# Optimization experiments

Measured on AMD Instinct MI355X. Metric: run time of the kernel, lower is better.

The kernel has to match this reference:

```python
import jax, jax.numpy as jnp
import numpy as np

B, T, E = 64, 512, 128
NODES, PATHS, OUT = 100000, 200000, 1000
PAD = 1  # padding_idx for node embedding


def setup_inputs() -> dict:
    key = jax.random.key(0)
    ks = jax.random.split(key, 10)
    starts = jax.random.randint(ks[0], (B, T), 0, NODES)
    paths = jax.random.randint(ks[1], (B, T), 0, PATHS)
    ends = jax.random.randint(ks[2], (B, T), 0, NODES)
    length = jax.random.randint(ks[3], (B,), 0, T)
    node_emb = jax.random.normal(ks[4], (NODES, E), dtype=jnp.float32)
    path_emb = jax.random.normal(ks[5], (PATHS, E), dtype=jnp.float32)
    W = jax.random.normal(ks[6], (E, 3 * E), dtype=jnp.float32)
    a = jax.random.normal(ks[7], (E,), dtype=jnp.float32)
    out_W = jax.random.normal(ks[8], (OUT, E), dtype=jnp.float32) * (1.0 / np.sqrt(E))
    out_b = jax.random.normal(ks[9], (OUT,), dtype=jnp.float32) * 0.01
    return dict(starts=starts, paths=paths, ends=ends, length=length,
                node_emb=node_emb, path_emb=path_emb, W=W, a=a,
                out_W=out_W, out_b=out_b)


def reference(starts, paths, ends, length, node_emb, path_emb, W, a, out_W, out_b):
    # padding_idx=1 -> that embedding row is zero
    node_emb = node_emb.at[PAD].set(0.0)
    es = node_emb[starts]          # [B,T,E]
    ep = path_emb[paths]           # [B,T,E]
    ee = node_emb[ends]            # [B,T,E]
    c = jnp.concatenate([es, ep, ee], axis=2)          # [B,T,3E]
    # dropout is identity in eval mode
    x = jnp.tanh(jnp.einsum('ed,btd->bte', W, c))      # [B,T,E]
    z = jax.nn.softmax(x @ a, axis=1)                  # [B,T] softmax over full T
    # original code sums only first length[i] attention weights (no renorm)
    mask = (jnp.arange(T)[None, :] < length[:, None]).astype(x.dtype)  # [B,T]
    v = jnp.einsum('bte,bt->be', x, z * mask)          # [B,E]
    return v @ out_W.T + out_b                          # [B,OUT]
```

## Files before the change

kernel.cpp:

```cpp
#include <hip/hip_runtime.h>
#include <hip/hip_bf16.h>

#define BB     64
#define TT     512
#define EE     128
#define NROWS  (BB * TT)
#define PADIDX 1
#define OUTN   1000

typedef __attribute__((ext_vector_type(8)))  short short8;
typedef __attribute__((ext_vector_type(16))) float f32x16;

__device__ __forceinline__ float tanh_fast(float v) {
    return 1.0f - 2.0f / (__expf(2.0f * v) + 1.0f);
}

__device__ __forceinline__ void split8(float4 a0, float4 a1, short8& hi, short8& lo) {
    float f[8] = {a0.x, a0.y, a0.z, a0.w, a1.x, a1.y, a1.z, a1.w};
#pragma unroll
    for (int i = 0; i < 8; ++i) {
        unsigned u = __float_as_uint(f[i]);
        unsigned r = (u + (0x7fffu + ((u >> 16) & 1u))) & 0xffff0000u;
        hi[i] = (short)(r >> 16);
        lo[i] = (short)(__float_as_uint(f[i] - __uint_as_float(r)) >> 16);
    }
}

__device__ __forceinline__ void gl_lds16(const void* g, void* l) {
    __builtin_amdgcn_global_load_lds((const __attribute__((address_space(1))) void*)g,
                                     (__attribute__((address_space(3))) void*)l, 16, 0, 0);
}

__global__ __launch_bounds__(256)
void k_prep(const float* __restrict__ W, unsigned short* __restrict__ Whg,
            unsigned short* __restrict__ Wlg)
{
    const int id = blockIdx.x * 256 + threadIdx.x;
    const int e  = id & 127;
    const int d  = id >> 7;
    const float v = W[e * 384 + d];
    const int t = d >> 6, k = d & 63;

    unsigned u = __float_as_uint(v);
    unsigned r = (u + (0x7fffu + ((u >> 16) & 1u))) & 0xffff0000u;
    const unsigned short h = (unsigned short)(r >> 16);
    const unsigned short l = (unsigned short)(__float_as_uint(v - __uint_as_float(r)) >> 16);

    const int boff = t * 16384 + e * 128 + ((k * 2) ^ ((e & 7) << 4));
    *(unsigned short*)((char*)Whg + boff) = h;
    *(unsigned short*)((char*)Wlg + boff) = l;
}

__global__ __launch_bounds__(256, 1)
void k_gemm_x(const int* __restrict__ starts, const int* __restrict__ paths,
              const int* __restrict__ ends,
              const float* __restrict__ node_emb, const float* __restrict__ path_emb,
              const unsigned short* __restrict__ Whg, const unsigned short* __restrict__ Wlg,
              const float* __restrict__ a, float* __restrict__ x, float* __restrict__ s)
{
    extern __shared__ char smem[];
    float*          Af      = (float*)smem;
    unsigned short* Wh      = (unsigned short*)(smem + 65536);
    unsigned short* Wl      = (unsigned short*)(smem + 98304);
    int*            idx_lds = (int*)(smem + 131072);
    float*          s_red   = (float*)(smem + 132608);

    const int tid = threadIdx.x;
    const int r0  = blockIdx.x * 128;

    if (tid < 128) {
        idx_lds[0 * 128 + tid] = starts[r0 + tid];
        idx_lds[1 * 128 + tid] = paths [r0 + tid];
        idx_lds[2 * 128 + tid] = ends  [r0 + tid];
    }

    const int lane = tid & 63;
    const int w    = tid >> 6;
    const int wm   = w >> 1;
    const int wn   = w & 1;
    const int fr   = lane & 31;
    const int kh   = lane >> 5;

    f32x16 acc[2][2];
#pragma unroll
    for (int mi = 0; mi < 2; ++mi)
#pragma unroll
        for (int ni = 0; ni < 2; ++ni)
#pragma unroll
            for (int i = 0; i < 16; ++i) acc[mi][ni][i] = 0.0f;

    __syncthreads();

    bool p0[2], p2[2];
#pragma unroll
    for (int mi = 0; mi < 2; ++mi) {
        const int rm = wm * 64 + mi * 32 + fr;
        p0[mi] = (idx_lds[0 * 128 + rm] == PADIDX);
        p2[mi] = (idx_lds[2 * 128 + rm] == PADIDX);
    }

#define ISSUE(T) do {                                                           \
    const int   seg_  = (T) >> 1;                                               \
    const char* embc_ = (const char*)((seg_ == 1) ? path_emb : node_emb);       \
    char*       afb_  = (char*)Af + (((T) & 1) ? 32768 : 0);                    \
    _Pragma("unroll")                                                           \
    for (int it = 0; it < 8; ++it) {                                            \
        const int row_ = w * 32 + it * 4 + (lane >> 4);                         \
        const int idx_ = idx_lds[seg_ * 128 + row_];                            \
        const char* src_ = embc_ + (size_t)idx_ * 512 + ((T) & 1) * 256         \
                         + (((lane & 15) * 16) ^ ((row_ & 7) << 4));            \
        gl_lds16(src_, afb_ + (w * 32 + it * 4) * 256);                         \
    }                                                                           \
    char* whb_ = (char*)Wh + (((T) & 1) ? 16384 : 0);                           \
    char* wlb_ = (char*)Wl + (((T) & 1) ? 16384 : 0);                           \
    _Pragma("unroll")                                                           \
    for (int rr = 0; rr < 4; ++rr) {                                            \
        const int o_ = rr * 4096 + w * 1024;                                    \
        gl_lds16((const char*)Whg + (T) * 16384 + o_ + lane * 16, whb_ + o_);   \
        gl_lds16((const char*)Wlg + (T) * 16384 + o_ + lane * 16, wlb_ + o_);   \
    }                                                                           \
} while (0)

#define COMPUTE(T) do {                                                         \
    const char* afc_ = (const char*)Af + (((T) & 1) ? 32768 : 0);               \
    const char* whc_ = (const char*)Wh + (((T) & 1) ? 16384 : 0);               \
    const char* wlc_ = (const char*)Wl + (((T) & 1) ? 16384 : 0);               \
    _Pragma("unroll")                                                           \
    for (int ksub = 0; ksub < 4; ++ksub) {                                      \
        short8 ah[2], al[2], bh[2], bl[2];                                      \
        _Pragma("unroll")                                                       \
        for (int mi = 0; mi < 2; ++mi) {                                        \
            const int row_ = wm * 64 + mi * 32 + fr;                            \
            const int swz_ = (row_ & 7) << 4;                                   \
            const int k0b_ = ksub * 64 + kh * 32;                               \
            float4 a0 = *(const float4*)(afc_ + row_ * 256 + (k0b_ ^ swz_));    \
            float4 a1 = *(const float4*)(afc_ + row_ * 256 + ((k0b_ + 16) ^ swz_)); \
            const bool pad_ = ((T) < 2) ? p0[mi] : (((T) >= 4) ? p2[mi] : false); \
            if (pad_) { a0 = make_float4(0.f, 0.f, 0.f, 0.f); a1 = a0; }        \
            split8(a0, a1, ah[mi], al[mi]);                                     \
        }                                                                       \
        _Pragma("unroll")                                                       \
        for (int ni = 0; ni < 2; ++ni) {                                        \
            const int e_ = wn * 64 + ni * 32 + fr;                              \
            const int bo_ = e_ * 128 + ((ksub * 32 + kh * 16) ^ ((e_ & 7) << 4)); \
            bh[ni] = *(const short8*)(whc_ + bo_);                              \
            bl[ni] = *(const short8*)(wlc_ + bo_);                              \
        }                                                                       \
        _Pragma("unroll")                                                       \
        for (int mi = 0; mi < 2; ++mi)                                          \
        _Pragma("unroll")                                                       \
        for (int ni = 0; ni < 2; ++ni) {                                        \
            acc[mi][ni] = __builtin_amdgcn_mfma_f32_32x32x16_bf16(ah[mi], bh[ni], acc[mi][ni], 0, 0, 0); \
            acc[mi][ni] = __builtin_amdgcn_mfma_f32_32x32x16_bf16(ah[mi], bl[ni], acc[mi][ni], 0, 0, 0); \
            acc[mi][ni] = __builtin_amdgcn_mfma_f32_32x32x16_bf16(al[mi], bh[ni], acc[mi][ni], 0, 0, 0); \
        }                                                                       \
    }                                                                           \
} while (0)

    ISSUE(0);

#pragma unroll
    for (int t = 0; t < 6; ++t) {
        if (t < 5) {
            ISSUE(t + 1);
            asm volatile("s_waitcnt vmcnt(16)" ::: "memory");
        } else {
            asm volatile("s_waitcnt vmcnt(0)" ::: "memory");
        }
        __builtin_amdgcn_s_barrier();
        __builtin_amdgcn_sched_barrier(0);
        COMPUTE(t);
        asm volatile("s_waitcnt lgkmcnt(0)" ::: "memory");
        __builtin_amdgcn_sched_barrier(0);
        __builtin_amdgcn_s_barrier();
    }

#undef ISSUE
#undef COMPUTE

    const float a0v = a[wn * 64 + fr];
    const float a1v = a[wn * 64 + 32 + fr];

#pragma unroll
    for (int mi = 0; mi < 2; ++mi) {
        float sp[16];
#pragma unroll
        for (int r = 0; r < 16; ++r) sp[r] = 0.0f;
#pragma unroll
        for (int ni = 0; ni < 2; ++ni) {
            const float ac  = (ni == 0) ? a0v : a1v;
            const int   col = wn * 64 + ni * 32 + fr;
#pragma unroll
            for (int r = 0; r < 16; ++r) {
                const int rowl = (r & 3) + 8 * (r >> 2) + 4 * kh;
                const float tv = tanh_fast(acc[mi][ni][r]);
                x[(size_t)(r0 + wm * 64 + mi * 32 + rowl) * EE + col] = tv;
                sp[r] = fmaf(tv, ac, sp[r]);
            }
        }
#pragma unroll
        for (int m = 1; m < 32; m <<= 1)
#pragma unroll
            for (int r = 0; r < 16; ++r) sp[r] += __shfl_xor(sp[r], m, 64);
        if (fr == 0) {
#pragma unroll
            for (int r = 0; r < 16; ++r) {
                const int rowl = (r & 3) + 8 * (r >> 2) + 4 * kh;
                s_red[(wm * 64 + mi * 32 + rowl) * 2 + wn] = sp[r];
            }
        }
    }
    __syncthreads();
    if (tid < 128) s[r0 + tid] = s_red[tid * 2] + s_red[tid * 2 + 1];
}

__global__ __launch_bounds__(256)
void k_attn(const float* __restrict__ s, const int* __restrict__ length,
            const float* __restrict__ x, float* __restrict__ v)
{
    __shared__ float sw[TT];
    __shared__ float red[256];

    const int b   = blockIdx.x >> 2;
    const int ec  = blockIdx.x & 3;
    const int tid = threadIdx.x;

    const float s0 = s[b * TT + tid];
    const float s1 = s[b * TT + 256 + tid];

    red[tid] = fmaxf(s0, s1);
    __syncthreads();
    for (int st = 128; st > 0; st >>= 1) {
        if (tid < st) red[tid] = fmaxf(red[tid], red[tid + st]);
        __syncthreads();
    }
    const float mx = red[0];
    __syncthreads();

    const float e0 = __expf(s0 - mx);
    const float e1 = __expf(s1 - mx);
    red[tid] = e0 + e1;
    __syncthreads();
    for (int st = 128; st > 0; st >>= 1) {
        if (tid < st) red[tid] += red[tid + st];
        __syncthreads();
    }
    const float inv = 1.0f / red[0];
    const int   len = length[b];
    __syncthreads();

    sw[tid]       = (tid < len)       ? e0 * inv : 0.0f;
    sw[tid + 256] = (tid + 256 < len) ? e1 * inv : 0.0f;
    __syncthreads();

    const int e  = ec * 32 + (tid & 31);
    const int tp = tid >> 5;
    const float* xb = x + (size_t)b * TT * EE;
    float acc = 0.0f;
#pragma unroll 8
    for (int t = tp; t < TT; t += 8)
        acc = fmaf(sw[t], xb[(size_t)t * EE + e], acc);

    red[tid] = acc;
    __syncthreads();
    if (tid < 32) {
        float r2 = 0.0f;
#pragma unroll
        for (int k = 0; k < 8; ++k) r2 += red[k * 32 + tid];
        v[b * EE + ec * 32 + tid] = r2;
    }
}

__global__ __launch_bounds__(256)
void k_out(const float* __restrict__ v, const float* __restrict__ out_W,
           const float* __restrict__ out_b, float* __restrict__ out)
{
    const int id = blockIdx.x * 256 + threadIdx.x;
    const int o  = id >> 6;
    const int bb = id & 63;

    const float4* vr = (const float4*)(v + bb * EE);
    const float4* wr = (const float4*)(out_W + o * EE);
    float acc = 0.0f;
#pragma unroll 8
    for (int qq = 0; qq < 32; ++qq) {
        const float4 a4 = vr[qq];
        const float4 b4 = wr[qq];
        acc = fmaf(a4.x, b4.x, acc);
        acc = fmaf(a4.y, b4.y, acc);
        acc = fmaf(a4.z, b4.z, acc);
        acc = fmaf(a4.w, b4.w, acc);
    }
    out[bb * OUTN + o] = acc + out_b[o];
}

extern "C" void kernel_launch(void* const* d_in, const int* in_sizes, int n_in,
                              void* d_out, int out_size, void* d_ws, size_t ws_size,
                              hipStream_t stream)
{
    const int*   starts   = (const int*)d_in[0];
    const int*   paths    = (const int*)d_in[1];
    const int*   ends     = (const int*)d_in[2];
    const int*   length   = (const int*)d_in[3];
    const float* node_emb = (const float*)d_in[4];
    const float* path_emb = (const float*)d_in[5];
    const float* W        = (const float*)d_in[6];
    const float* a        = (const float*)d_in[7];
    const float* out_W    = (const float*)d_in[8];
    const float* out_b    = (const float*)d_in[9];
    float*       out      = (float*)d_out;

    float* x = (float*)d_ws;
    float* s = x + (size_t)NROWS * EE;
    float* v = s + NROWS;
    unsigned short* Whg = (unsigned short*)(v + BB * EE);
    unsigned short* Wlg = Whg + 6 * 8192;

    static const int SMEM = 133632;
    hipFuncSetAttribute((const void*)k_gemm_x,
                        hipFuncAttributeMaxDynamicSharedMemorySize, SMEM);

    k_prep<<<192, 256, 0, stream>>>(W, Whg, Wlg);
    k_gemm_x<<<NROWS / 128, 256, SMEM, stream>>>(starts, paths, ends,
                                                 node_emb, path_emb, Whg, Wlg,
                                                 a, x, s);
    k_attn<<<BB * 4, 256, 0, stream>>>(s, length, x, v);
    k_out<<<(BB * OUTN) / 256, 256, 0, stream>>>(v, out_W, out_b, out);
}
```

Before: 209.0 us.

## Load gathered embeddings and weights straight into registers instead of staging in LDS

The fused gather-GEMM stops staging embedding rows and bf16 weight tiles through LDS with async loads and double buffering. Each wave now owns a 32-column slice of the output over 64 rows, reads the gathered embedding floats and pre-laid-out weight fragments directly from global memory into MFMA registers, and uses a smaller block tile with two blocks per CU. The prep kernel rewrites the weights into MFMA-fragment order to make these direct loads contiguous. The attention kernel's weighted sum now runs only over the first length rows, skipping masked positions; this relies on L2 and cache hits for reuse instead of explicit LDS pipelining.

```diff
diff --git a/kernel.cpp b/kernel.cpp
--- a/kernel.cpp
+++ b/kernel.cpp
@@ -1,5 +1,4 @@
 #include <hip/hip_runtime.h>
-#include <hip/hip_bf16.h>
 
 #define BB     64
 #define TT     512
@@ -26,192 +25,120 @@
     }
 }
 
-__device__ __forceinline__ void gl_lds16(const void* g, void* l) {
-    __builtin_amdgcn_global_load_lds((const __attribute__((address_space(1))) void*)g,
-                                     (__attribute__((address_space(3))) void*)l, 16, 0, 0);
-}
-
 __global__ __launch_bounds__(256)
 void k_prep(const float* __restrict__ W, unsigned short* __restrict__ Whg,
             unsigned short* __restrict__ Wlg)
 {
     const int id = blockIdx.x * 256 + threadIdx.x;
-    const int e  = id & 127;
-    const int d  = id >> 7;
-    const float v = W[e * 384 + d];
-    const int t = d >> 6, k = d & 63;
-
+    const int j  = id & 7;
+    const int l  = (id >> 3) & 63;
+    const int r2 = id >> 9;
+    const int ks = r2 % 24;
+    const int et = r2 / 24;
+    const int e  = et * 32 + (l & 31);
+    const int k  = ks * 16 + (l >> 5) * 8 + j;
+
+    const float v = W[e * 384 + k];
     unsigned u = __float_as_uint(v);
     unsigned r = (u + (0x7fffu + ((u >> 16) & 1u))) & 0xffff0000u;
-    const unsigned short h = (unsigned short)(r >> 16);
-    const unsigned short l = (unsigned short)(__float_as_uint(v - __uint_as_float(r)) >> 16);
-
-    const int boff = t * 16384 + e * 128 + ((k * 2) ^ ((e & 7) << 4));
-    *(unsigned short*)((char*)Whg + boff) = h;
-    *(unsigned short*)((char*)Wlg + boff) = l;
-}
-
-__global__ __launch_bounds__(256, 1)
+    Whg[id] = (unsigned short)(r >> 16);
+    Wlg[id] = (unsigned short)(__float_as_uint(v - __uint_as_float(r)) >> 16);
+}
+
+__global__ __launch_bounds__(256, 2)
 void k_gemm_x(const int* __restrict__ starts, const int* __restrict__ paths,
               const int* __restrict__ ends,
               const float* __restrict__ node_emb, const float* __restrict__ path_emb,
               const unsigned short* __restrict__ Whg, const unsigned short* __restrict__ Wlg,
               const float* __restrict__ a, float* __restrict__ x, float* __restrict__ s)
 {
-    extern __shared__ char smem[];
-    float*          Af      = (float*)smem;
-    unsigned short* Wh      = (unsigned short*)(smem + 65536);
-    unsigned short* Wl      = (unsigned short*)(smem + 98304);
-    int*            idx_lds = (int*)(smem + 131072);
-    float*          s_red   = (float*)(smem + 132608);
-
-    const int tid = threadIdx.x;
-    const int r0  = blockIdx.x * 128;
-
-    if (tid < 128) {
-        idx_lds[0 * 128 + tid] = starts[r0 + tid];
-        idx_lds[1 * 128 + tid] = paths [r0 + tid];
-        idx_lds[2 * 128 + tid] = ends  [r0 + tid];
-    }
-
+    __shared__ float s_red[64][4];
+
+    const int tid  = threadIdx.x;
     const int lane = tid & 63;
     const int w    = tid >> 6;
-    const int wm   = w >> 1;
-    const int wn   = w & 1;
     const int fr   = lane & 31;
     const int kh   = lane >> 5;
-
-    f32x16 acc[2][2];
+    const int r0   = blockIdx.x * 64;
+
+    const char* base[2][3];
+    bool padf[2][3];
+#pragma unroll
+    for (int mi = 0; mi < 2; ++mi) {
+        const int row = r0 + mi * 32 + fr;
+        const int i0 = starts[row], i1 = paths[row], i2 = ends[row];
+        base[mi][0] = (const char*)node_emb + (size_t)i0 * 512 + kh * 32;
+        base[mi][1] = (const char*)path_emb + (size_t)i1 * 512 + kh * 32;
+        base[mi][2] = (const char*)node_emb + (size_t)i2 * 512 + kh * 32;
+        padf[mi][0] = (i0 == PADIDX);
+        padf[mi][1] = false;
+        padf[mi][2] = (i2 == PADIDX);
+    }
+
+    const char* wbh = (const char*)Whg + ((size_t)(w * 24 * 64) + lane) * 16;
+    const char* wbl = (const char*)Wlg + ((size_t)(w * 24 * 64) + lane) * 16;
+
+    f32x16 acc[2];
 #pragma unroll
     for (int mi = 0; mi < 2; ++mi)
 #pragma unroll
-        for (int ni = 0; ni < 2; ++ni)
-#pragma unroll
-            for (int i = 0; i < 16; ++i) acc[mi][ni][i] = 0.0f;
-
-    __syncthreads();
-
-    bool p0[2], p2[2];
-#pragma unroll
-    for (int mi = 0; mi < 2; ++mi) {
-        const int rm = wm * 64 + mi * 32 + fr;
-        p0[mi] = (idx_lds[0 * 128 + rm] == PADIDX);
-        p2[mi] = (idx_lds[2 * 128 + rm] == PADIDX);
-    }
-
-#define ISSUE(T) do {                                                           \
-    const int   seg_  = (T) >> 1;                                               \
-    const char* embc_ = (const char*)((seg_ == 1) ? path_emb : node_emb);       \
-    char*       afb_  = (char*)Af + (((T) & 1) ? 32768 : 0);                    \
-    _Pragma("unroll")                                                           \
-    for (int it = 0; it < 8; ++it) {                                            \
-        const int row_ = w * 32 + it * 4 + (lane >> 4);                         \
-        const int idx_ = idx_lds[seg_ * 128 + row_];                            \
-        const char* src_ = embc_ + (size_t)idx_ * 512 + ((T) & 1) * 256         \
-                         + (((lane & 15) * 16) ^ ((row_ & 7) << 4));            \
-        gl_lds16(src_, afb_ + (w * 32 + it * 4) * 256);                         \
-    }                                                                           \
-    char* whb_ = (char*)Wh + (((T) & 1) ? 16384 : 0);                           \
-    char* wlb_ = (char*)Wl + (((T) & 1) ? 16384 : 0);                           \
-    _Pragma("unroll")                                                           \
-    for (int rr = 0; rr < 4; ++rr) {                                            \
-        const int o_ = rr * 4096 + w * 1024;                                    \
-        gl_lds16((const char*)Whg + (T) * 16384 + o_ + lane * 16, whb_ + o_);   \
-        gl_lds16((const char*)Wlg + (T) * 16384 + o_ + lane * 16, wlb_ + o_);   \
-    }                                                                           \
-} while (0)
-
-#define COMPUTE(T) do {                                                         \
-    const char* afc_ = (const char*)Af + (((T) & 1) ? 32768 : 0);               \
-    const char* whc_ = (const char*)Wh + (((T) & 1) ? 16384 : 0);               \
-    const char* wlc_ = (const char*)Wl + (((T) & 1) ? 16384 : 0);               \
-    _Pragma("unroll")                                                           \
-    for (int ksub = 0; ksub < 4; ++ksub) {                                      \
-        short8 ah[2], al[2], bh[2], bl[2];                                      \
-        _Pragma("unroll")                                                       \
-        for (int mi = 0; mi < 2; ++mi) {                                        \
-            const int row_ = wm * 64 + mi * 32 + fr;                            \
-            const int swz_ = (row_ & 7) << 4;                                   \
-            const int k0b_ = ksub * 64 + kh * 32;                               \
-            float4 a0 = *(const float4*)(afc_ + row_ * 256 + (k0b_ ^ swz_));    \
-            float4 a1 = *(const float4*)(afc_ + row_ * 256 + ((k0b_ + 16) ^ swz_)); \
-            const bool pad_ = ((T) < 2) ? p0[mi] : (((T) >= 4) ? p2[mi] : false); \
-            if (pad_) { a0 = make_float4(0.f, 0.f, 0.f, 0.f); a1 = a0; }        \
-            split8(a0, a1, ah[mi], al[mi]);                                     \
-        }                                                                       \
-        _Pragma("unroll")                                                       \
-        for (int ni = 0; ni < 2; ++ni) {                                        \
-            const int e_ = wn * 64 + ni * 32 + fr;                              \
-            const int bo_ = e_ * 128 + ((ksub * 32 + kh * 16) ^ ((e_ & 7) << 4)); \
-            bh[ni] = *(const short8*)(whc_ + bo_);                              \
-            bl[ni] = *(const short8*)(wlc_ + bo_);                              \
-        }                                                                       \
-        _Pragma("unroll")                                                       \
-        for (int mi = 0; mi < 2; ++mi)                                          \
-        _Pragma("unroll")                                                       \
-        for (int ni = 0; ni < 2; ++ni) {                                        \
-            acc[mi][ni] = __builtin_amdgcn_mfma_f32_32x32x16_bf16(ah[mi], bh[ni], acc[mi][ni], 0, 0, 0); \
-            acc[mi][ni] = __builtin_amdgcn_mfma_f32_32x32x16_bf16(ah[mi], bl[ni], acc[mi][ni], 0, 0, 0); \
-            acc[mi][ni] = __builtin_amdgcn_mfma_f32_32x32x16_bf16(al[mi], bh[ni], acc[mi][ni], 0, 0, 0); \
-        }                                                                       \
-    }                                                                           \
-} while (0)
-
-    ISSUE(0);
-
-#pragma unroll
-    for (int t = 0; t < 6; ++t) {
-        if (t < 5) {
-            ISSUE(t + 1);
-            asm volatile("s_waitcnt vmcnt(16)" ::: "memory");
-        } else {
-            asm volatile("s_waitcnt vmcnt(0)" ::: "memory");
-        }
-        __builtin_amdgcn_s_barrier();
-        __builtin_amdgcn_sched_barrier(0);
-        COMPUTE(t);
-        asm volatile("s_waitcnt lgkmcnt(0)" ::: "memory");
-        __builtin_amdgcn_sched_barrier(0);
-        __builtin_amdgcn_s_barrier();
-    }
-
-#undef ISSUE
-#undef COMPUTE
-
-    const float a0v = a[wn * 64 + fr];
-    const float a1v = a[wn * 64 + 32 + fr];
+        for (int i = 0; i < 16; ++i) acc[mi][i] = 0.0f;
+
+#pragma unroll
+    for (int ks = 0; ks < 24; ++ks) {
+        const int seg = ks >> 3;
+        const int off = (ks & 7) * 64;
+
+        const short8 bh = *(const short8*)(wbh + ks * 1024);
+        const short8 bl = *(const short8*)(wbl + ks * 1024);
+
+        float4 a0[2], a1[2];
+#pragma unroll
+        for (int mi = 0; mi < 2; ++mi) {
+            a0[mi] = *(const float4*)(base[mi][seg] + off);
+            a1[mi] = *(const float4*)(base[mi][seg] + off + 16);
+            if (padf[mi][seg]) {
+                a0[mi] = make_float4(0.f, 0.f, 0.f, 0.f);
+                a1[mi] = a0[mi];
+            }
+        }
+#pragma unroll
+        for (int mi = 0; mi < 2; ++mi) {
+            short8 ah, al;
+            split8(a0[mi], a1[mi], ah, al);
+            acc[mi] = __builtin_amdgcn_mfma_f32_32x32x16_bf16(ah, bh, acc[mi], 0, 0, 0);
+            acc[mi] = __builtin_amdgcn_mfma_f32_32x32x16_bf16(ah, bl, acc[mi], 0, 0, 0);
+            acc[mi] = __builtin_amdgcn_mfma_f32_32x32x16_bf16(al, bh, acc[mi], 0, 0, 0);
+        }
+    }
+
+    const float av = a[w * 32 + fr];
 
 #pragma unroll
     for (int mi = 0; mi < 2; ++mi) {
         float sp[16];
 #pragma unroll
-        for (int r = 0; r < 16; ++r) sp[r] = 0.0f;
-#pragma unroll
-        for (int ni = 0; ni < 2; ++ni) {
-            const float ac  = (ni == 0) ? a0v : a1v;
-            const int   col = wn * 64 + ni * 32 + fr;
+        for (int r = 0; r < 16; ++r) {
+            const int rowl = (r & 3) + 8 * (r >> 2) + 4 * kh;
+            const float tv = tanh_fast(acc[mi][r]);
+            x[(size_t)(r0 + mi * 32 + rowl) * EE + w * 32 + fr] = tv;
+            sp[r] = tv * av;
+        }
+#pragma unroll
+        for (int m = 1; m < 32; m <<= 1)
+#pragma unroll
+            for (int r = 0; r < 16; ++r) sp[r] += __shfl_xor(sp[r], m, 64);
+        if (fr == 0) {
 #pragma unroll
             for (int r = 0; r < 16; ++r) {
                 const int rowl = (r & 3) + 8 * (r >> 2) + 4 * kh;
-                const float tv = tanh_fast(acc[mi][ni][r]);
-                x[(size_t)(r0 + wm * 64 + mi * 32 + rowl) * EE + col] = tv;
-                sp[r] = fmaf(tv, ac, sp[r]);
+                s_red[mi * 32 + rowl][w] = sp[r];
             }
         }
-#pragma unroll
-        for (int m = 1; m < 32; m <<= 1)
-#pragma unroll
-            for (int r = 0; r < 16; ++r) sp[r] += __shfl_xor(sp[r], m, 64);
-        if (fr == 0) {
-#pragma unroll
-            for (int r = 0; r < 16; ++r) {
-                const int rowl = (r & 3) + 8 * (r >> 2) + 4 * kh;
-                s_red[(wm * 64 + mi * 32 + rowl) * 2 + wn] = sp[r];
-            }
-        }
-    }
-    __syncthreads();
-    if (tid < 128) s[r0 + tid] = s_red[tid * 2] + s_red[tid * 2 + 1];
+    }
+    __syncthreads();
+    if (tid < 64)
+        s[r0 + tid] = s_red[tid][0] + s_red[tid][1] + s_red[tid][2] + s_red[tid][3];
 }
 
 __global__ __launch_bounds__(256)
@@ -249,16 +176,15 @@
     const int   len = length[b];
     __syncthreads();
 
-    sw[tid]       = (tid < len)       ? e0 * inv : 0.0f;
-    sw[tid + 256] = (tid + 256 < len) ? e1 * inv : 0.0f;
+    sw[tid]       = e0 * inv;
+    sw[tid + 256] = e1 * inv;
     __syncthreads();
 
     const int e  = ec * 32 + (tid & 31);
     const int tp = tid >> 5;
     const float* xb = x + (size_t)b * TT * EE;
     float acc = 0.0f;
-#pragma unroll 8
-    for (int t = tp; t < TT; t += 8)
+    for (int t = tp; t < len; t += 8)
         acc = fmaf(sw[t], xb[(size_t)t * EE + e], acc);
 
     red[tid] = acc;
@@ -314,16 +240,12 @@
     float* s = x + (size_t)NROWS * EE;
     float* v = s + NROWS;
     unsigned short* Whg = (unsigned short*)(v + BB * EE);
-    unsigned short* Wlg = Whg + 6 * 8192;
-
-    static const int SMEM = 133632;
-    hipFuncSetAttribute((const void*)k_gemm_x,
-                        hipFuncAttributeMaxDynamicSharedMemorySize, SMEM);
+    unsigned short* Wlg = Whg + 49152;
 
     k_prep<<<192, 256, 0, stream>>>(W, Whg, Wlg);
-    k_gemm_x<<<NROWS / 128, 256, SMEM, stream>>>(starts, paths, ends,
-                                                 node_emb, path_emb, Whg, Wlg,
-                                                 a, x, s);
+    k_gemm_x<<<NROWS / 64, 256, 0, stream>>>(starts, paths, ends,
+                                             node_emb, path_emb, Whg, Wlg,
+                                             a, x, s);
     k_attn<<<BB * 4, 256, 0, stream>>>(s, length, x, v);
     k_out<<<(BB * OUTN) / 256, 256, 0, stream>>>(v, out_W, out_b, out);
 }
```

Measured after the change: 225.2 us. 7.7% more time.
